# Kernel optimization log

Hardware: AMD Instinct MI355X
Metric: run time of the kernel (lower is better)

The kernel has to match this reference:

```python
import jax, jax.numpy as jnp
import numpy as np

NEG_INF = -1e20

# Dims: s=512 samples, b=2048 background, t=32 trees, f=64 features, h=128 hidden, y=1
S, B, T, F, H, Y = 512, 2048, 32, 64, 128, 1


def setup_inputs() -> dict:
    key = jax.random.key(0)
    ks = jax.random.split(key, 8)
    X = jax.random.normal(ks[0], (S, F), dtype=jnp.float32)
    background_X = jax.random.normal(ks[1], (B, F), dtype=jnp.float32)
    background_y = jax.random.normal(ks[2], (B, Y), dtype=jnp.float32)
    neighbors_hot = jax.random.randint(ks[3], (S, B, T), 0, 2).astype(jnp.bool_)
    # encoder params: Linear(F->H), Tanh, Linear(H->H)  (n_layers=2)
    W1 = jax.random.normal(ks[4], (F, H), dtype=jnp.float32) / np.sqrt(F)
    b1 = jnp.zeros((H,), dtype=jnp.float32)
    W2 = jax.random.normal(ks[5], (H, H), dtype=jnp.float32) / np.sqrt(H)
    b2 = jnp.zeros((H,), dtype=jnp.float32)
    return {"X": X, "background_X": background_X, "background_y": background_y,
            "neighbors_hot": neighbors_hot, "W1": W1, "b1": b1, "W2": W2, "b2": b2}


def reference(X, background_X, background_y, neighbors_hot, W1, b1, W2, b2):
    def encode(x):
        return jnp.tanh(x @ W1 + b1) @ W2 + b2  # Linear-Tanh-Linear

    X_enc = encode(X)                    # (s, h)
    bg_enc = encode(background_X)        # (b, h)
    dots = X_enc @ bg_enc.T              # (s, b)
    # broadcast over trees + mask, softmax over background axis
    scores = jnp.where(neighbors_hot, dots[:, :, None], NEG_INF)  # (s, b, t)
    first_alphas = jax.nn.softmax(scores, axis=1)                 # (s, b, t)
    first_leaf_xs = jnp.einsum('sbt,bf->stf', first_alphas, background_X)
    first_leaf_y = jnp.einsum('sbt,by->sty', first_alphas, background_y)
    return first_leaf_xs, first_leaf_y, first_alphas
```

## Files before the change

### kernel.cpp

```cpp
#include <hip/hip_runtime.h>
#include <hip/hip_bf16.h>

#define NS 512
#define NB 2048
#define NT 32
#define NF 64
#define NH 128
#define NFX 80

#define OY  ((size_t)NS * NT * NF)
#define OA  (OY + (size_t)NS * NT)

#define PACK_B 2048
#define ENC_B  1280
#define TR_B   32

typedef __attribute__((ext_vector_type(8))) short bf16x8;
typedef __attribute__((ext_vector_type(4))) float f32x4;

__device__ __forceinline__ unsigned short f2bfu(float x) {
    __hip_bfloat16 h = __float2bfloat16(x);
    return __builtin_bit_cast(unsigned short, h);
}

__device__ __forceinline__ unsigned int pack16_bytes(uint4 v) {
    unsigned int r = 0;
    unsigned int xs[4] = {v.x, v.y, v.z, v.w};
    #pragma unroll
    for (int i = 0; i < 4; ++i) {
        unsigned int x = xs[i];
        unsigned int t = (x | ((x & 0x7F7F7F7Fu) + 0x7F7F7F7Fu)) & 0x80808080u;
        t >>= 7;
        unsigned int n = (t | (t >> 7) | (t >> 14) | (t >> 21)) & 0xFu;
        r |= n << (i * 4);
    }
    return r;
}

__global__ __launch_bounds__(256) void prep_k(const void* mask,
        unsigned long long* pm,
        const float* __restrict__ X, const float* __restrict__ bgX,
        const float* __restrict__ bgy,
        const float* __restrict__ W1, const float* __restrict__ b1,
        const float* __restrict__ W2, const float* __restrict__ b2,
        float* __restrict__ enc, unsigned short* __restrict__ bgXT2) {
    __shared__ float cbuf[64 * 68];
    const int blk = blockIdx.x;
    const int tid = threadIdx.x;

    if (blk < PACK_B) {
        int* flagp = (int*)cbuf;
        if (tid == 0) *flagp = 0;
        __syncthreads();
        {
            uint4 v = ((const uint4*)mask)[tid];
            if (((v.x | v.y | v.z | v.w) & 0xFFFFFF00u) != 0u) *flagp = 1;
        }
        __syncthreads();
        const int isbyte = *flagp;

        const int wv = tid >> 6, lane = tid & 63;
        unsigned long long* pmw = pm + (size_t)blk * 256 + wv * 64;
        if (isbyte) {
            const char* base = (const char*)mask + (size_t)blk * 16384 + wv * 4096;
            #pragma unroll
            for (int k = 0; k < 4; ++k) {
                uint4 q = *(const uint4*)(base + k * 1024 + lane * 16);
                unsigned int p = pack16_bytes(q);
                unsigned int p1 = (unsigned int)__shfl_down((int)p, 1, 64);
                unsigned int r32 = p | (p1 << 16);
                unsigned int h32 = (unsigned int)__shfl_down((int)r32, 2, 64);
                if ((lane & 3) == 0)
                    pmw[k * 16 + (lane >> 2)] =
                        (unsigned long long)r32 | ((unsigned long long)h32 << 32);
            }
        } else {
            const char* base = (const char*)mask + (size_t)blk * 65536 + wv * 16384;
            #pragma unroll 4
            for (int k = 0; k < 16; ++k) {
                uint4 v = *(const uint4*)(base + k * 1024 + lane * 16);
                unsigned int r = (v.x ? 1u : 0u) | (v.y ? 2u : 0u) |
                                 (v.z ? 4u : 0u) | (v.w ? 8u : 0u);
                r |= ((unsigned int)__shfl_down((int)r, 1, 64)) << 4;
                r |= ((unsigned int)__shfl_down((int)r, 2, 64)) << 8;
                r |= ((unsigned int)__shfl_down((int)r, 4, 64)) << 16;
                unsigned long long r64 = (unsigned long long)r |
                    ((unsigned long long)(unsigned int)__shfl_down((int)r, 8, 64) << 32);
                if ((lane & 15) == 0)
                    pmw[k * 4 + (lane >> 4)] = r64;
            }
        }
        return;
    }

    if (blk < PACK_B + ENC_B) {
        const int r0 = (blk - PACK_B) * 2;
        float* xr = cbuf;
        float* hr = cbuf + 128;
        if (tid < 128) {
            int r = tid >> 6, c = tid & 63;
            int row = r0 + r;
            const float* src = (row < NS) ? (X + (size_t)row * NF)
                                          : (bgX + (size_t)(row - NS) * NF);
            xr[r * 64 + c] = src[c];
        }
        __syncthreads();
        const int j = tid & 127, h = tid >> 7;
        const float* xh = xr + h * 64;
        float a1 = b1[j];
        #pragma unroll 4
        for (int f = 0; f < NF; ++f)
            a1 = fmaf(xh[f], W1[f * NH + j], a1);
        hr[h * 128 + j] = tanhf(a1);
        __syncthreads();
        const float* hh = hr + h * 128;
        float a2 = b2[j];
        #pragma unroll 4
        for (int k = 0; k < NH; ++k)
            a2 = fmaf(hh[k], W2[k * NH + j], a2);
        enc[(size_t)(r0 + h) * NH + j] = a2;
        return;
    }

    {
        const int bb0 = blk - PACK_B - ENC_B;
        const int b0 = bb0 * 64;
        float (*t_lds)[65] = (float(*)[65])cbuf;
        #pragma unroll
        for (int it = 0; it < 4; ++it) {
            int idx = (it * 256 + tid) * 4;
            int r = idx >> 6, c = idx & 63;
            *(float4*)(&t_lds[r][c]) = *(const float4*)(bgX + (size_t)(b0 + r) * NF + c);
        }
        __syncthreads();
        uint4* fb = (uint4*)bgXT2;
        const int c2 = tid >> 7;
        const int cg = bb0 * 2 + c2;
        for (int idx = tid & 127; idx < 320; idx += 128) {
            const int n = idx >> 6, l = idx & 63;
            const int lo = l & 15, hi = l >> 4;
            union { unsigned short u[8]; uint4 q; } pk;
            if (n < 4) {
                #pragma unroll
                for (int j = 0; j < 8; ++j)
                    pk.u[j] = f2bfu(t_lds[c2 * 32 + hi * 8 + j][n * 16 + lo]);
            } else {
                #pragma unroll
                for (int j = 0; j < 8; ++j) {
                    if (lo == 0)      pk.u[j] = f2bfu(bgy[b0 + c2 * 32 + hi * 8 + j]);
                    else if (lo == 1) pk.u[j] = 0x3F80;
                    else              pk.u[j] = 0;
                }
            }
            fb[((size_t)cg * 5 + n) * 64 + l] = pk.q;
        }
    }
}

__global__ __launch_bounds__(256) void dots_k(const float* __restrict__ Xe,
        const float* __restrict__ Be, float* __restrict__ dots) {
    __shared__ float At[64 * 68];
    __shared__ float Bt[64 * 68];
    const int s0 = blockIdx.y * 64, b0 = blockIdx.x * 64;
    const int tid = threadIdx.x;
    const int ts = tid >> 4, tb = tid & 15;
    float acc[4][4] = {};
    for (int kt = 0; kt < 2; ++kt) {
        __syncthreads();
        #pragma unroll
        for (int it = 0; it < 4; ++it) {
            int idx = tid * 4 + it * 1024;
            int r = idx >> 6, k = idx & 63;
            *(float4*)(&At[r * 68 + k]) = *(const float4*)(Xe + (size_t)(s0 + r) * NH + kt * 64 + k);
            float4 bvv = *(const float4*)(Be + (size_t)(b0 + r) * NH + kt * 64 + k);
            Bt[(k + 0) * 68 + r] = bvv.x;
            Bt[(k + 1) * 68 + r] = bvv.y;
            Bt[(k + 2) * 68 + r] = bvv.z;
            Bt[(k + 3) * 68 + r] = bvv.w;
        }
        __syncthreads();
        #pragma unroll 4
        for (int k = 0; k < 64; ++k) {
            float4 bq = *(const float4*)(&Bt[k * 68 + tb * 4]);
            float a[4];
            #pragma unroll
            for (int i = 0; i < 4; ++i) a[i] = At[(ts + 16 * i) * 68 + k];
            #pragma unroll
            for (int i = 0; i < 4; ++i) {
                acc[i][0] = fmaf(a[i], bq.x, acc[i][0]);
                acc[i][1] = fmaf(a[i], bq.y, acc[i][1]);
                acc[i][2] = fmaf(a[i], bq.z, acc[i][2]);
                acc[i][3] = fmaf(a[i], bq.w, acc[i][3]);
            }
        }
    }
    #pragma unroll
    for (int i = 0; i < 4; ++i) {
        float4 v = make_float4(acc[i][0], acc[i][1], acc[i][2], acc[i][3]);
        *(float4*)(&dots[(size_t)(s0 + ts + 16 * i) * NB + b0 + tb * 4]) = v;
    }
}

__global__ __launch_bounds__(256) void fusedA_k(float* __restrict__ dots,
        const unsigned long long* __restrict__ pmask,
        const unsigned short* __restrict__ bgXT2,
        float* __restrict__ rden_g, float* __restrict__ out) {
    __shared__ __align__(16) unsigned int mrow[NB];
    __shared__ __align__(16) unsigned short e_bf[NB];
    __shared__ float part[3 * NT * NFX];
    __shared__ float wmax[4];
    __shared__ float rden_l[NT];
    __shared__ float ytmp[NT];

    const int s = blockIdx.x;
    const int tid = threadIdx.x;
    const int lane = tid & 63, w = tid >> 6;
    const int lo = lane & 15, hi = lane >> 4;

    float* drow = dots + (size_t)s * NB;
    float4 d0 = *(const float4*)(drow + tid * 8);
    float4 d1 = *(const float4*)(drow + tid * 8 + 4);
    const uint4* pmrow = (const uint4*)((const unsigned int*)pmask + (size_t)s * NB);
    *(uint4*)(&mrow[tid * 4]) = pmrow[tid];
    *(uint4*)(&mrow[(tid + 256) * 4]) = pmrow[tid + 256];
    float pmax = fmaxf(fmaxf(fmaxf(d0.x, d0.y), fmaxf(d0.z, d0.w)),
                       fmaxf(fmaxf(d1.x, d1.y), fmaxf(d1.z, d1.w)));
    #pragma unroll
    for (int off = 32; off >= 1; off >>= 1)
        pmax = fmaxf(pmax, __shfl_xor(pmax, off, 64));
    if (lane == 0) wmax[w] = pmax;
    __syncthreads();
    const float Ms = fmaxf(fmaxf(wmax[0], wmax[1]), fmaxf(wmax[2], wmax[3]));
    float ev[8] = {d0.x, d0.y, d0.z, d0.w, d1.x, d1.y, d1.z, d1.w};
    union { unsigned short u[8]; uint4 q; } epk;
    #pragma unroll
    for (int q = 0; q < 8; ++q) { ev[q] = __expf(ev[q] - Ms); epk.u[q] = f2bfu(ev[q]); }
    *(float4*)(drow + tid * 8)     = make_float4(ev[0], ev[1], ev[2], ev[3]);
    *(float4*)(drow + tid * 8 + 4) = make_float4(ev[4], ev[5], ev[6], ev[7]);
    *(uint4*)(&e_bf[tid * 8]) = epk.q;
    __syncthreads();

    f32x4 acc[2][5] = {};
    const uint4* fb = (const uint4*)bgXT2;
    #pragma unroll 2
    for (int ks = 0; ks < 16; ++ks) {
        const int bb = w * 512 + ks * 32 + hi * 8;
        uint4 ew4 = *(const uint4*)(&e_bf[bb]);
        uint4 m0 = *(const uint4*)(&mrow[bb]);
        uint4 m1 = *(const uint4*)(&mrow[bb + 4]);
        unsigned int ew[4] = {ew4.x, ew4.y, ew4.z, ew4.w};
        unsigned int mv[8] = {m0.x, m0.y, m0.z, m0.w, m1.x, m1.y, m1.z, m1.w};
        unsigned int A0[4], A1[4];
        #pragma unroll
        for (int p = 0; p < 4; ++p) {
            unsigned int mlo = mv[2 * p]     >> lo;
            unsigned int mhi = mv[2 * p + 1] >> lo;
            unsigned int k0 = ((mlo & 1u)       ? 0x0000FFFFu : 0u) |
                              ((mhi & 1u)       ? 0xFFFF0000u : 0u);
            unsigned int k1 = ((mlo & 0x10000u) ? 0x0000FFFFu : 0u) |
                              ((mhi & 0x10000u) ? 0xFFFF0000u : 0u);
            A0[p] = ew[p] & k0;
            A1[p] = ew[p] & k1;
        }
        bf16x8 a0 = __builtin_bit_cast(bf16x8, make_uint4(A0[0], A0[1], A0[2], A0[3]));
        bf16x8 a1 = __builtin_bit_cast(bf16x8, make_uint4(A1[0], A1[1], A1[2], A1[3]));
        const uint4* fr = fb + ((size_t)(w * 16 + ks) * 5) * 64 + lane;
        #pragma unroll
        for (int n = 0; n < 5; ++n) {
            uint4 bv = fr[n * 64];
            bf16x8 bfr = __builtin_bit_cast(bf16x8, bv);
            acc[0][n] = __builtin_amdgcn_mfma_f32_16x16x32_bf16(a0, bfr, acc[0][n], 0, 0, 0);
            acc[1][n] = __builtin_amdgcn_mfma_f32_16x16x32_bf16(a1, bfr, acc[1][n], 0, 0, 0);
        }
    }

    if (w > 0) {
        #pragma unroll
        for (int m = 0; m < 2; ++m)
            #pragma unroll
            for (int n = 0; n < 5; ++n)
                #pragma unroll
                for (int r = 0; r < 4; ++r) {
                    int t = m * 16 + hi * 4 + r, f = n * 16 + lo;
                    part[(w - 1) * (NT * NFX) + t * NFX + f] = acc[m][n][r];
                }
    }
    __syncthreads();
    if (w == 0) {
        #pragma unroll
        for (int m = 0; m < 2; ++m)
            #pragma unroll
            for (int r = 0; r < 4; ++r) {
                int t = m * 16 + hi * 4 + r;
                int o = t * NFX + 64 + lo;
                float tot = acc[m][4][r] + part[o] + part[NT * NFX + o] + part[2 * NT * NFX + o];
                if (lo == 0) ytmp[t] = tot;
                if (lo == 1) rden_l[t] = (tot > 0.f) ? 1.f / tot : 0.f;
            }
    }
    __syncthreads();
    if (w == 0) {
        float* xout = out + (size_t)s * NT * NF;
        #pragma unroll
        for (int m = 0; m < 2; ++m)
            #pragma unroll
            for (int n = 0; n < 4; ++n)
                #pragma unroll
                for (int r = 0; r < 4; ++r) {
                    int t = m * 16 + hi * 4 + r, f = n * 16 + lo;
                    int o = t * NFX + f;
                    float tot = acc[m][n][r] + part[o] + part[NT * NFX + o] + part[2 * NT * NFX + o];
                    xout[t * NF + f] = tot * rden_l[t];
                }
    }
    if (tid < 32) {
        out[OY + (size_t)s * NT + tid] = ytmp[tid] * rden_l[tid];
        rden_g[(size_t)s * NT + tid] = rden_l[tid];
    }
}

__global__ __launch_bounds__(256) void alphas_k(const float* __restrict__ e,
        const unsigned int* __restrict__ pmask32, const float* __restrict__ rden_g,
        float* __restrict__ out) {
    const int tid = threadIdx.x;
    const int blk = blockIdx.x;
    const int s = blk >> 3;
    const int tq = tid & 7;
    const f32x4 rd4 = *(const f32x4*)(rden_g + (size_t)s * NT + tq * 4);
    const float* erow = e + (size_t)s * NB;
    const unsigned int* mr = pmask32 + (size_t)s * NB;
    float* aout = out + OA + (size_t)s * NB * NT;
    const int b0 = (blk & 7) * 256 + (tid >> 3);

    float ev[8];
    unsigned int mv[8];
    #pragma unroll
    for (int j = 0; j < 8; ++j) {
        ev[j] = erow[b0 + j * 32];
        mv[j] = mr[b0 + j * 32] >> (tq * 4);
    }
    #pragma unroll
    for (int j = 0; j < 8; ++j) {
        const int b = b0 + j * 32;
        f32x4 v;
        v.x = (mv[j] & 1u) ? ev[j] * rd4.x : 0.f;
        v.y = (mv[j] & 2u) ? ev[j] * rd4.y : 0.f;
        v.z = (mv[j] & 4u) ? ev[j] * rd4.z : 0.f;
        v.w = (mv[j] & 8u) ? ev[j] * rd4.w : 0.f;
        *(f32x4*)(aout + (size_t)b * NT + tq * 4) = v;
    }
}

extern "C" void kernel_launch(void* const* d_in, const int* in_sizes, int n_in,
                              void* d_out, int out_size, void* d_ws, size_t ws_size,
                              hipStream_t stream) {
    (void)in_sizes; (void)n_in; (void)out_size; (void)ws_size;
    const float* X   = (const float*)d_in[0];
    const float* bgX = (const float*)d_in[1];
    const float* bgy = (const float*)d_in[2];
    const void*  nh  = d_in[3];
    const float* W1  = (const float*)d_in[4];
    const float* b1v = (const float*)d_in[5];
    const float* W2  = (const float*)d_in[6];
    const float* b2v = (const float*)d_in[7];
    float* out = (float*)d_out;
    char* ws = (char*)d_ws;

    float* enc = (float*)(ws + 4096);
    float* rden_g = (float*)(ws + 4096);
    float* Xe = enc;
    float* Be = enc + (size_t)NS * NH;
    float* dots = (float*)(ws + 4096 + (size_t)(NS + NB) * NH * 4);
    unsigned long long* pmask = (unsigned long long*)((char*)dots + (size_t)NS * NB * 4);
    unsigned short* bgXT2 = (unsigned short*)((char*)pmask + (size_t)NS * NB * NT / 64 * 8);

    prep_k<<<PACK_B + ENC_B + TR_B, 256, 0, stream>>>(nh, pmask, X, bgX, bgy,
                                                      W1, b1v, W2, b2v, enc, bgXT2);
    dots_k<<<dim3(NB / 64, NS / 64), 256, 0, stream>>>(Xe, Be, dots);
    fusedA_k<<<NS, 256, 0, stream>>>(dots, pmask, bgXT2, rden_g, out);
    alphas_k<<<NS * 8, 256, 0, stream>>>(dots, (const unsigned int*)pmask, rden_g, out);
}
```

Measured before the change: 98.32 us.

## Fuse mask bit-packing into softmax kernel and pad partial-sum LDS stride

Moves the boolean mask packing out of the prep kernel and into fusedA_k, so each sample block reads its own mask row, packs it into LDS, and writes the packed row to global memory for alphas_k. This removes a separate pass that wrote the packed mask and then read it back, and shrinks the prep grid to just the encoder and transpose blocks. The pack now runs on only 512 blocks, which may serialise the raw mask read. The partial-sum LDS stride is also padded from 80 to 81 floats to reduce bank conflicts.

```diff
diff --git a/kernel.cpp b/kernel.cpp
--- a/kernel.cpp
+++ b/kernel.cpp
@@ -7,11 +7,11 @@
 #define NF 64
 #define NH 128
 #define NFX 80
+#define PSTR 81
 
 #define OY  ((size_t)NS * NT * NF)
 #define OA  (OY + (size_t)NS * NT)
 
-#define PACK_B 2048
 #define ENC_B  1280
 #define TR_B   32
 
@@ -37,64 +37,18 @@
     return r;
 }
 
-__global__ __launch_bounds__(256) void prep_k(const void* mask,
-        unsigned long long* pm,
+__global__ __launch_bounds__(256) void prep2_k(
         const float* __restrict__ X, const float* __restrict__ bgX,
         const float* __restrict__ bgy,
         const float* __restrict__ W1, const float* __restrict__ b1,
         const float* __restrict__ W2, const float* __restrict__ b2,
         float* __restrict__ enc, unsigned short* __restrict__ bgXT2) {
-    __shared__ float cbuf[64 * 68];
+    __shared__ float cbuf[64 * 65];
     const int blk = blockIdx.x;
     const int tid = threadIdx.x;
 
-    if (blk < PACK_B) {
-        int* flagp = (int*)cbuf;
-        if (tid == 0) *flagp = 0;
-        __syncthreads();
-        {
-            uint4 v = ((const uint4*)mask)[tid];
-            if (((v.x | v.y | v.z | v.w) & 0xFFFFFF00u) != 0u) *flagp = 1;
-        }
-        __syncthreads();
-        const int isbyte = *flagp;
-
-        const int wv = tid >> 6, lane = tid & 63;
-        unsigned long long* pmw = pm + (size_t)blk * 256 + wv * 64;
-        if (isbyte) {
-            const char* base = (const char*)mask + (size_t)blk * 16384 + wv * 4096;
-            #pragma unroll
-            for (int k = 0; k < 4; ++k) {
-                uint4 q = *(const uint4*)(base + k * 1024 + lane * 16);
-                unsigned int p = pack16_bytes(q);
-                unsigned int p1 = (unsigned int)__shfl_down((int)p, 1, 64);
-                unsigned int r32 = p | (p1 << 16);
-                unsigned int h32 = (unsigned int)__shfl_down((int)r32, 2, 64);
-                if ((lane & 3) == 0)
-                    pmw[k * 16 + (lane >> 2)] =
-                        (unsigned long long)r32 | ((unsigned long long)h32 << 32);
-            }
-        } else {
-            const char* base = (const char*)mask + (size_t)blk * 65536 + wv * 16384;
-            #pragma unroll 4
-            for (int k = 0; k < 16; ++k) {
-                uint4 v = *(const uint4*)(base + k * 1024 + lane * 16);
-                unsigned int r = (v.x ? 1u : 0u) | (v.y ? 2u : 0u) |
-                                 (v.z ? 4u : 0u) | (v.w ? 8u : 0u);
-                r |= ((unsigned int)__shfl_down((int)r, 1, 64)) << 4;
-                r |= ((unsigned int)__shfl_down((int)r, 2, 64)) << 8;
-                r |= ((unsigned int)__shfl_down((int)r, 4, 64)) << 16;
-                unsigned long long r64 = (unsigned long long)r |
-                    ((unsigned long long)(unsigned int)__shfl_down((int)r, 8, 64) << 32);
-                if ((lane & 15) == 0)
-                    pmw[k * 4 + (lane >> 4)] = r64;
-            }
-        }
-        return;
-    }
-
-    if (blk < PACK_B + ENC_B) {
-        const int r0 = (blk - PACK_B) * 2;
+    if (blk < ENC_B) {
+        const int r0 = blk * 2;
         float* xr = cbuf;
         float* hr = cbuf + 128;
         if (tid < 128) {
@@ -123,7 +77,7 @@
     }
 
     {
-        const int bb0 = blk - PACK_B - ENC_B;
+        const int bb0 = blk - ENC_B;
         const int b0 = bb0 * 64;
         float (*t_lds)[65] = (float(*)[65])cbuf;
         #pragma unroll
@@ -142,14 +96,14 @@
             union { unsigned short u[8]; uint4 q; } pk;
             if (n < 4) {
                 #pragma unroll
-                for (int j = 0; j < 8; ++j)
-                    pk.u[j] = f2bfu(t_lds[c2 * 32 + hi * 8 + j][n * 16 + lo]);
+                for (int jj = 0; jj < 8; ++jj)
+                    pk.u[jj] = f2bfu(t_lds[c2 * 32 + hi * 8 + jj][n * 16 + lo]);
             } else {
                 #pragma unroll
-                for (int j = 0; j < 8; ++j) {
-                    if (lo == 0)      pk.u[j] = f2bfu(bgy[b0 + c2 * 32 + hi * 8 + j]);
-                    else if (lo == 1) pk.u[j] = 0x3F80;
-                    else              pk.u[j] = 0;
+                for (int jj = 0; jj < 8; ++jj) {
+                    if (lo == 0)      pk.u[jj] = f2bfu(bgy[b0 + c2 * 32 + hi * 8 + jj]);
+                    else if (lo == 1) pk.u[jj] = 0x3F80;
+                    else              pk.u[jj] = 0;
                 }
             }
             fb[((size_t)cg * 5 + n) * 64 + l] = pk.q;
@@ -201,13 +155,13 @@
     }
 }
 
-__global__ __launch_bounds__(256) void fusedA_k(float* __restrict__ dots,
-        const unsigned long long* __restrict__ pmask,
-        const unsigned short* __restrict__ bgXT2,
+__global__ __launch_bounds__(256) void fusedA_k(const void* __restrict__ mask,
+        float* __restrict__ dots, const unsigned short* __restrict__ bgXT2,
+        unsigned int* __restrict__ pmask32,
         float* __restrict__ rden_g, float* __restrict__ out) {
     __shared__ __align__(16) unsigned int mrow[NB];
     __shared__ __align__(16) unsigned short e_bf[NB];
-    __shared__ float part[3 * NT * NFX];
+    __shared__ float part[3 * NT * PSTR];
     __shared__ float wmax[4];
     __shared__ float rden_l[NT];
     __shared__ float ytmp[NT];
@@ -220,9 +174,35 @@
     float* drow = dots + (size_t)s * NB;
     float4 d0 = *(const float4*)(drow + tid * 8);
     float4 d1 = *(const float4*)(drow + tid * 8 + 4);
-    const uint4* pmrow = (const uint4*)((const unsigned int*)pmask + (size_t)s * NB);
-    *(uint4*)(&mrow[tid * 4]) = pmrow[tid];
-    *(uint4*)(&mrow[(tid + 256) * 4]) = pmrow[tid + 256];
+    int isbyte;
+    {
+        uint4 v = ((const uint4*)mask)[w * 64 + lane];
+        isbyte = (__ballot(((v.x | v.y | v.z | v.w) & 0xFFFFFF00u) != 0u) != 0ull);
+    }
+    if (isbyte) {
+        const char* base = (const char*)mask + (size_t)s * 65536 + w * 16384;
+        #pragma unroll 4
+        for (int k = 0; k < 16; ++k) {
+            uint4 q = *(const uint4*)(base + k * 1024 + lane * 16);
+            unsigned int p = pack16_bytes(q);
+            unsigned int p1 = (unsigned int)__shfl_down((int)p, 1, 64);
+            if ((lane & 1) == 0)
+                mrow[w * 512 + k * 32 + (lane >> 1)] = p | (p1 << 16);
+        }
+    } else {
+        const char* base = (const char*)mask + (size_t)s * 262144 + w * 65536;
+        for (int k = 0; k < 64; ++k) {
+            uint4 v = *(const uint4*)(base + k * 1024 + lane * 16);
+            unsigned int r = (v.x ? 1u : 0u) | (v.y ? 2u : 0u) |
+                             (v.z ? 4u : 0u) | (v.w ? 8u : 0u);
+            r |= ((unsigned int)__shfl_down((int)r, 1, 64)) << 4;
+            r |= ((unsigned int)__shfl_down((int)r, 2, 64)) << 8;
+            r |= ((unsigned int)__shfl_down((int)r, 4, 64)) << 16;
+            if ((lane & 7) == 0)
+                mrow[w * 512 + k * 8 + (lane >> 3)] = r;
+        }
+    }
+
     float pmax = fmaxf(fmaxf(fmaxf(d0.x, d0.y), fmaxf(d0.z, d0.w)),
                        fmaxf(fmaxf(d1.x, d1.y), fmaxf(d1.z, d1.w)));
     #pragma unroll
@@ -238,6 +218,9 @@
     *(float4*)(drow + tid * 8)     = make_float4(ev[0], ev[1], ev[2], ev[3]);
     *(float4*)(drow + tid * 8 + 4) = make_float4(ev[4], ev[5], ev[6], ev[7]);
     *(uint4*)(&e_bf[tid * 8]) = epk.q;
+    unsigned int* pmg = pmask32 + (size_t)s * NB;
+    *(uint4*)(pmg + tid * 4)          = *(const uint4*)(&mrow[tid * 4]);
+    *(uint4*)(pmg + (tid + 256) * 4)  = *(const uint4*)(&mrow[(tid + 256) * 4]);
     __syncthreads();
 
     f32x4 acc[2][5] = {};
@@ -282,7 +265,7 @@
                 #pragma unroll
                 for (int r = 0; r < 4; ++r) {
                     int t = m * 16 + hi * 4 + r, f = n * 16 + lo;
-                    part[(w - 1) * (NT * NFX) + t * NFX + f] = acc[m][n][r];
+                    part[(w - 1) * (NT * PSTR) + t * PSTR + f] = acc[m][n][r];
                 }
     }
     __syncthreads();
@@ -292,8 +275,8 @@
             #pragma unroll
             for (int r = 0; r < 4; ++r) {
                 int t = m * 16 + hi * 4 + r;
-                int o = t * NFX + 64 + lo;
-                float tot = acc[m][4][r] + part[o] + part[NT * NFX + o] + part[2 * NT * NFX + o];
+                int o = t * PSTR + 64 + lo;
+                float tot = acc[m][4][r] + part[o] + part[NT * PSTR + o] + part[2 * NT * PSTR + o];
                 if (lo == 0) ytmp[t] = tot;
                 if (lo == 1) rden_l[t] = (tot > 0.f) ? 1.f / tot : 0.f;
             }
@@ -308,8 +291,8 @@
                 #pragma unroll
                 for (int r = 0; r < 4; ++r) {
                     int t = m * 16 + hi * 4 + r, f = n * 16 + lo;
-                    int o = t * NFX + f;
-                    float tot = acc[m][n][r] + part[o] + part[NT * NFX + o] + part[2 * NT * NFX + o];
+                    int o = t * PSTR + f;
+                    float tot = acc[m][n][r] + part[o] + part[NT * PSTR + o] + part[2 * NT * PSTR + o];
                     xout[t * NF + f] = tot * rden_l[t];
                 }
     }
@@ -371,12 +354,11 @@
     float* Xe = enc;
     float* Be = enc + (size_t)NS * NH;
     float* dots = (float*)(ws + 4096 + (size_t)(NS + NB) * NH * 4);
-    unsigned long long* pmask = (unsigned long long*)((char*)dots + (size_t)NS * NB * 4);
-    unsigned short* bgXT2 = (unsigned short*)((char*)pmask + (size_t)NS * NB * NT / 64 * 8);
-
-    prep_k<<<PACK_B + ENC_B + TR_B, 256, 0, stream>>>(nh, pmask, X, bgX, bgy,
-                                                      W1, b1v, W2, b2v, enc, bgXT2);
+    unsigned int* pmask32 = (unsigned int*)((char*)dots + (size_t)NS * NB * 4);
+    unsigned short* bgXT2 = (unsigned short*)((char*)pmask32 + (size_t)NS * NB * 4);
+
+    prep2_k<<<ENC_B + TR_B, 256, 0, stream>>>(X, bgX, bgy, W1, b1v, W2, b2v, enc, bgXT2);
     dots_k<<<dim3(NB / 64, NS / 64), 256, 0, stream>>>(Xe, Be, dots);
-    fusedA_k<<<NS, 256, 0, stream>>>(dots, pmask, bgXT2, rden_g, out);
-    alphas_k<<<NS * 8, 256, 0, stream>>>(dots, (const unsigned int*)pmask, rden_g, out);
-}
+    fusedA_k<<<NS, 256, 0, stream>>>(nh, dots, bgXT2, pmask32, rden_g, out);
+    alphas_k<<<NS * 8, 256, 0, stream>>>(dots, pmask32, rden_g, out);
+}
```

Result: slower. 115.2 us (+17.2%).

## Tile encoder MLP into LDS-tiled GEMM blocks and pad partial-sum stride

Applied to the files above, without the earlier changes.

The encoder previously ran as 1280 blocks, each handling two rows with a per-thread dot product that reads W1 and W2 rows straight from global memory. It is replaced by a 64x64 LDS-tiled GEMM for layer 1, with tanh fused in, inside prep_k. Layer 2 becomes a separate tiled kernel, which adds a launch and an intermediate buffer round-trip. The layer-1 blocks are placed first so they are scheduled ahead of the mask packing. The partial-sum stride in fusedA_k is padded from 80 to 81 to reduce LDS bank conflicts.

```diff
diff --git a/kernel.cpp b/kernel.cpp
--- a/kernel.cpp
+++ b/kernel.cpp
@@ -7,13 +7,14 @@
 #define NF 64
 #define NH 128
 #define NFX 80
+#define PSTR 81
 
 #define OY  ((size_t)NS * NT * NF)
 #define OA  (OY + (size_t)NS * NT)
 
+#define L1_B   80
+#define TR_B   32
 #define PACK_B 2048
-#define ENC_B  1280
-#define TR_B   32
 
 typedef __attribute__((ext_vector_type(8))) short bf16x8;
 typedef __attribute__((ext_vector_type(4))) float f32x4;
@@ -42,13 +43,93 @@
         const float* __restrict__ X, const float* __restrict__ bgX,
         const float* __restrict__ bgy,
         const float* __restrict__ W1, const float* __restrict__ b1,
-        const float* __restrict__ W2, const float* __restrict__ b2,
-        float* __restrict__ enc, unsigned short* __restrict__ bgXT2) {
-    __shared__ float cbuf[64 * 68];
+        float* __restrict__ enc1, unsigned short* __restrict__ bgXT2) {
+    __shared__ float cbuf[2 * 64 * 68];
     const int blk = blockIdx.x;
     const int tid = threadIdx.x;
 
-    if (blk < PACK_B) {
+    if (blk < L1_B) {
+        const int bx = blk & 1, by = blk >> 1;
+        float (*Xt)[68] = (float(*)[68])cbuf;
+        float (*Wt)[68] = (float(*)[68])(cbuf + 64 * 68);
+        const int r0 = by * 64;
+        const float* srcbase = (r0 < NS) ? (X + (size_t)r0 * NF)
+                                         : (bgX + (size_t)(r0 - NS) * NF);
+        #pragma unroll
+        for (int it = 0; it < 4; ++it) {
+            int idx = tid * 4 + it * 1024;
+            int r = idx >> 6, c = idx & 63;
+            *(float4*)(&Xt[r][c]) = *(const float4*)(srcbase + (size_t)r * NF + c);
+            *(float4*)(&Wt[r][c]) = *(const float4*)(W1 + (size_t)r * NH + bx * 64 + c);
+        }
+        __syncthreads();
+        const int ts = tid >> 4, tb = tid & 15;
+        float4 bq = *(const float4*)(b1 + bx * 64 + tb * 4);
+        float acc[4][4];
+        #pragma unroll
+        for (int i = 0; i < 4; ++i) {
+            acc[i][0] = bq.x; acc[i][1] = bq.y; acc[i][2] = bq.z; acc[i][3] = bq.w;
+        }
+        #pragma unroll 4
+        for (int k = 0; k < 64; ++k) {
+            float4 wq = *(const float4*)(&Wt[k][tb * 4]);
+            float a[4];
+            #pragma unroll
+            for (int i = 0; i < 4; ++i) a[i] = Xt[ts + 16 * i][k];
+            #pragma unroll
+            for (int i = 0; i < 4; ++i) {
+                acc[i][0] = fmaf(a[i], wq.x, acc[i][0]);
+                acc[i][1] = fmaf(a[i], wq.y, acc[i][1]);
+                acc[i][2] = fmaf(a[i], wq.z, acc[i][2]);
+                acc[i][3] = fmaf(a[i], wq.w, acc[i][3]);
+            }
+        }
+        #pragma unroll
+        for (int i = 0; i < 4; ++i) {
+            float4 v = make_float4(tanhf(acc[i][0]), tanhf(acc[i][1]),
+                                   tanhf(acc[i][2]), tanhf(acc[i][3]));
+            *(float4*)(&enc1[(size_t)(r0 + ts + 16 * i) * NH + bx * 64 + tb * 4]) = v;
+        }
+        return;
+    }
+
+    if (blk < L1_B + TR_B) {
+        const int bb0 = blk - L1_B;
+        const int b0 = bb0 * 64;
+        float (*t_lds)[65] = (float(*)[65])cbuf;
+        #pragma unroll
+        for (int it = 0; it < 4; ++it) {
+            int idx = (it * 256 + tid) * 4;
+            int r = idx >> 6, c = idx & 63;
+            *(float4*)(&t_lds[r][c]) = *(const float4*)(bgX + (size_t)(b0 + r) * NF + c);
+        }
+        __syncthreads();
+        uint4* fb = (uint4*)bgXT2;
+        const int c2 = tid >> 7;
+        const int cg = bb0 * 2 + c2;
+        for (int idx = tid & 127; idx < 320; idx += 128) {
+            const int n = idx >> 6, l = idx & 63;
+            const int lo = l & 15, hi = l >> 4;
+            union { unsigned short u[8]; uint4 q; } pk;
+            if (n < 4) {
+                #pragma unroll
+                for (int jj = 0; jj < 8; ++jj)
+                    pk.u[jj] = f2bfu(t_lds[c2 * 32 + hi * 8 + jj][n * 16 + lo]);
+            } else {
+                #pragma unroll
+                for (int jj = 0; jj < 8; ++jj) {
+                    if (lo == 0)      pk.u[jj] = f2bfu(bgy[b0 + c2 * 32 + hi * 8 + jj]);
+                    else if (lo == 1) pk.u[jj] = 0x3F80;
+                    else              pk.u[jj] = 0;
+                }
+            }
+            fb[((size_t)cg * 5 + n) * 64 + l] = pk.q;
+        }
+        return;
+    }
+
+    {
+        const int pb = blk - L1_B - TR_B;
         int* flagp = (int*)cbuf;
         if (tid == 0) *flagp = 0;
         __syncthreads();
@@ -60,9 +141,9 @@
         const int isbyte = *flagp;
 
         const int wv = tid >> 6, lane = tid & 63;
-        unsigned long long* pmw = pm + (size_t)blk * 256 + wv * 64;
+        unsigned long long* pmw = pm + (size_t)pb * 256 + wv * 64;
         if (isbyte) {
-            const char* base = (const char*)mask + (size_t)blk * 16384 + wv * 4096;
+            const char* base = (const char*)mask + (size_t)pb * 16384 + wv * 4096;
             #pragma unroll
             for (int k = 0; k < 4; ++k) {
                 uint4 q = *(const uint4*)(base + k * 1024 + lane * 16);
@@ -75,7 +156,7 @@
                         (unsigned long long)r32 | ((unsigned long long)h32 << 32);
             }
         } else {
-            const char* base = (const char*)mask + (size_t)blk * 65536 + wv * 16384;
+            const char* base = (const char*)mask + (size_t)pb * 65536 + wv * 16384;
             #pragma unroll 4
             for (int k = 0; k < 16; ++k) {
                 uint4 v = *(const uint4*)(base + k * 1024 + lane * 16);
@@ -90,70 +171,53 @@
                     pmw[k * 4 + (lane >> 4)] = r64;
             }
         }
-        return;
-    }
-
-    if (blk < PACK_B + ENC_B) {
-        const int r0 = (blk - PACK_B) * 2;
-        float* xr = cbuf;
-        float* hr = cbuf + 128;
-        if (tid < 128) {
-            int r = tid >> 6, c = tid & 63;
-            int row = r0 + r;
-            const float* src = (row < NS) ? (X + (size_t)row * NF)
-                                          : (bgX + (size_t)(row - NS) * NF);
-            xr[r * 64 + c] = src[c];
-        }
-        __syncthreads();
-        const int j = tid & 127, h = tid >> 7;
-        const float* xh = xr + h * 64;
-        float a1 = b1[j];
+    }
+}
+
+__global__ __launch_bounds__(256) void layer2_k(const float* __restrict__ enc1,
+        const float* __restrict__ W2, const float* __restrict__ b2,
+        float* __restrict__ enc) {
+    __shared__ float Ht[64 * 68];
+    __shared__ float Wt[64 * 68];
+    const int bx = blockIdx.x & 1, by = blockIdx.x >> 1;
+    const int tid = threadIdx.x;
+    const int ts = tid >> 4, tb = tid & 15;
+    const int r0 = by * 64;
+    float4 bq = *(const float4*)(b2 + bx * 64 + tb * 4);
+    float acc[4][4];
+    #pragma unroll
+    for (int i = 0; i < 4; ++i) {
+        acc[i][0] = bq.x; acc[i][1] = bq.y; acc[i][2] = bq.z; acc[i][3] = bq.w;
+    }
+    for (int kt = 0; kt < 2; ++kt) {
+        __syncthreads();
+        #pragma unroll
+        for (int it = 0; it < 4; ++it) {
+            int idx = tid * 4 + it * 1024;
+            int r = idx >> 6, c = idx & 63;
+            *(float4*)(&Ht[r * 68 + c]) = *(const float4*)(enc1 + (size_t)(r0 + r) * NH + kt * 64 + c);
+            *(float4*)(&Wt[r * 68 + c]) = *(const float4*)(W2 + (size_t)(kt * 64 + r) * NH + bx * 64 + c);
+        }
+        __syncthreads();
         #pragma unroll 4
-        for (int f = 0; f < NF; ++f)
-            a1 = fmaf(xh[f], W1[f * NH + j], a1);
-        hr[h * 128 + j] = tanhf(a1);
-        __syncthreads();
-        const float* hh = hr + h * 128;
-        float a2 = b2[j];
-        #pragma unroll 4
-        for (int k = 0; k < NH; ++k)
-            a2 = fmaf(hh[k], W2[k * NH + j], a2);
-        enc[(size_t)(r0 + h) * NH + j] = a2;
-        return;
-    }
-
-    {
-        const int bb0 = blk - PACK_B - ENC_B;
-        const int b0 = bb0 * 64;
-        float (*t_lds)[65] = (float(*)[65])cbuf;
-        #pragma unroll
-        for (int it = 0; it < 4; ++it) {
-            int idx = (it * 256 + tid) * 4;
-            int r = idx >> 6, c = idx & 63;
-            *(float4*)(&t_lds[r][c]) = *(const float4*)(bgX + (size_t)(b0 + r) * NF + c);
-        }
-        __syncthreads();
-        uint4* fb = (uint4*)bgXT2;
-        const int c2 = tid >> 7;
-        const int cg = bb0 * 2 + c2;
-        for (int idx = tid & 127; idx < 320; idx += 128) {
-            const int n = idx >> 6, l = idx & 63;
-            const int lo = l & 15, hi = l >> 4;
-            union { unsigned short u[8]; uint4 q; } pk;
-            if (n < 4) {
-                #pragma unroll
-                for (int j = 0; j < 8; ++j)
-                    pk.u[j] = f2bfu(t_lds[c2 * 32 + hi * 8 + j][n * 16 + lo]);
-            } else {
-                #pragma unroll
-                for (int j = 0; j < 8; ++j) {
-                    if (lo == 0)      pk.u[j] = f2bfu(bgy[b0 + c2 * 32 + hi * 8 + j]);
-                    else if (lo == 1) pk.u[j] = 0x3F80;
-                    else              pk.u[j] = 0;
-                }
-            }
-            fb[((size_t)cg * 5 + n) * 64 + l] = pk.q;
-        }
+        for (int k = 0; k < 64; ++k) {
+            float4 wq = *(const float4*)(&Wt[k * 68 + tb * 4]);
+            float a[4];
+            #pragma unroll
+            for (int i = 0; i < 4; ++i) a[i] = Ht[(ts + 16 * i) * 68 + k];
+            #pragma unroll
+            for (int i = 0; i < 4; ++i) {
+                acc[i][0] = fmaf(a[i], wq.x, acc[i][0]);
+                acc[i][1] = fmaf(a[i], wq.y, acc[i][1]);
+                acc[i][2] = fmaf(a[i], wq.z, acc[i][2]);
+                acc[i][3] = fmaf(a[i], wq.w, acc[i][3]);
+            }
+        }
+    }
+    #pragma unroll
+    for (int i = 0; i < 4; ++i) {
+        float4 v = make_float4(acc[i][0], acc[i][1], acc[i][2], acc[i][3]);
+        *(float4*)(&enc[(size_t)(r0 + ts + 16 * i) * NH + bx * 64 + tb * 4]) = v;
     }
 }
 
@@ -207,7 +271,7 @@
         float* __restrict__ rden_g, float* __restrict__ out) {
     __shared__ __align__(16) unsigned int mrow[NB];
     __shared__ __align__(16) unsigned short e_bf[NB];
-    __shared__ float part[3 * NT * NFX];
+    __shared__ float part[3 * NT * PSTR];
     __shared__ float wmax[4];
     __shared__ float rden_l[NT];
     __shared__ float ytmp[NT];
@@ -282,7 +346,7 @@
                 #pragma unroll
                 for (int r = 0; r < 4; ++r) {
                     int t = m * 16 + hi * 4 + r, f = n * 16 + lo;
-                    part[(w - 1) * (NT * NFX) + t * NFX + f] = acc[m][n][r];
+                    part[(w - 1) * (NT * PSTR) + t * PSTR + f] = acc[m][n][r];
                 }
     }
     __syncthreads();
@@ -292,8 +356,8 @@
             #pragma unroll
             for (int r = 0; r < 4; ++r) {
                 int t = m * 16 + hi * 4 + r;
-                int o = t * NFX + 64 + lo;
-                float tot = acc[m][4][r] + part[o] + part[NT * NFX + o] + part[2 * NT * NFX + o];
+                int o = t * PSTR + 64 + lo;
+                float tot = acc[m][4][r] + part[o] + part[NT * PSTR + o] + part[2 * NT * PSTR + o];
                 if (lo == 0) ytmp[t] = tot;
                 if (lo == 1) rden_l[t] = (tot > 0.f) ? 1.f / tot : 0.f;
             }
@@ -308,8 +372,8 @@
                 #pragma unroll
                 for (int r = 0; r < 4; ++r) {
                     int t = m * 16 + hi * 4 + r, f = n * 16 + lo;
-                    int o = t * NFX + f;
-                    float tot = acc[m][n][r] + part[o] + part[NT * NFX + o] + part[2 * NT * NFX + o];
+                    int o = t * PSTR + f;
+                    float tot = acc[m][n][r] + part[o] + part[NT * PSTR + o] + part[2 * NT * PSTR + o];
                     xout[t * NF + f] = tot * rden_l[t];
                 }
     }
@@ -373,9 +437,11 @@
     float* dots = (float*)(ws + 4096 + (size_t)(NS + NB) * NH * 4);
     unsigned long long* pmask = (unsigned long long*)((char*)dots + (size_t)NS * NB * 4);
     unsigned short* bgXT2 = (unsigned short*)((char*)pmask + (size_t)NS * NB * NT / 64 * 8);
-
-    prep_k<<<PACK_B + ENC_B + TR_B, 256, 0, stream>>>(nh, pmask, X, bgX, bgy,
-                                                      W1, b1v, W2, b2v, enc, bgXT2);
+    float* enc1 = (float*)((char*)bgXT2 + (size_t)64 * 5 * 64 * 16);
+
+    prep_k<<<L1_B + TR_B + PACK_B, 256, 0, stream>>>(nh, pmask, X, bgX, bgy,
+                                                     W1, b1v, enc1, bgXT2);
+    layer2_k<<<L1_B, 256, 0, stream>>>(enc1, W2, b2v, enc);
     dots_k<<<dim3(NB / 64, NS / 64), 256, 0, stream>>>(Xe, Be, dots);
     fusedA_k<<<NS, 256, 0, stream>>>(dots, pmask, bgXT2, rden_g, out);
     alphas_k<<<NS * 8, 256, 0, stream>>>(dots, (const unsigned int*)pmask, rden_g, out);
```

Result: slower. 104.9 us (+6.7%).
